# Performance work log

Measured on AMD Instinct MI355X. Metric: run time of the kernel, lower is better.

Reference implementation:

```python
import jax, jax.numpy as jnp
import numpy as np

N_WIRES = 4
N_LAYERS = 2
B = 16384
EPS = 1e-5


def apply_ry(state, wire, theta):
    # state: (B,2,2,2,2) complex64; theta: scalar or (B,)
    st = jnp.moveaxis(state, wire + 1, 1)
    half = jnp.asarray(theta) * 0.5
    c = jnp.cos(half).reshape(-1, 1, 1, 1).astype(state.dtype)
    s = jnp.sin(half).reshape(-1, 1, 1, 1).astype(state.dtype)
    n0 = c * st[:, 0] - s * st[:, 1]
    n1 = s * st[:, 0] + c * st[:, 1]
    return jnp.moveaxis(jnp.stack([n0, n1], axis=1), 1, wire + 1)


def apply_rz(state, wire, theta):
    st = jnp.moveaxis(state, wire + 1, 1)
    half = jnp.asarray(theta) * 0.5
    c = jnp.cos(half)
    s = jnp.sin(half)
    p0 = (c - 1j * s).reshape(-1, 1, 1, 1).astype(state.dtype)
    p1 = (c + 1j * s).reshape(-1, 1, 1, 1).astype(state.dtype)
    return jnp.moveaxis(jnp.stack([p0 * st[:, 0], p1 * st[:, 1]], axis=1), 1, wire + 1)


def apply_cnot(state, ctrl, tgt):
    st = jnp.moveaxis(state, (ctrl + 1, tgt + 1), (1, 2))
    # flip target where control == 1
    st = jnp.concatenate([st[:, :1], st[:, 1:, ::-1]], axis=1)
    return jnp.moveaxis(st, (1, 2), (ctrl + 1, tgt + 1))


def expect_z(state):
    probs = jnp.real(state * jnp.conj(state))  # (B,2,2,2,2)
    exps = []
    for w in range(N_WIRES):
        p = jnp.moveaxis(probs, w + 1, 1)
        exps.append((p[:, 0] - p[:, 1]).sum(axis=(1, 2, 3)))
    return jnp.stack(exps, axis=-1)  # (B,4)


def quanv(x, qparams):
    bsz = x.shape[0]
    # 2x2 patches in row-major loop order: (B, 196, 4) with [p00,p01,p10,p11]
    patches = x.reshape(bsz, 14, 2, 14, 2).transpose(0, 1, 3, 2, 4).reshape(bsz, 196, 4)
    patches = jnp.transpose(patches, (1, 0, 2))  # (196, B, 4)
    state0 = jnp.zeros((bsz, 2, 2, 2, 2), jnp.complex64).at[:, 0, 0, 0, 0].set(1.0)

    def step(state, vals):
        # NOTE: original code never resets the device between patches -> state carries over
        for i in range(N_WIRES):
            state = apply_ry(state, i, vals[:, i])
        for l in range(N_LAYERS):
            for i in range(N_WIRES):
                state = apply_ry(state, i, qparams[l, i, 0])
                state = apply_rz(state, i, qparams[l, i, 1])
            for i in range(N_WIRES - 1):
                state = apply_cnot(state, i, i + 1)
        return state, expect_z(state)

    _, meas = jax.lax.scan(step, state0, patches)  # (196, B, 4)
    return jnp.transpose(meas, (1, 0, 2)).reshape(bsz, 196 * 4)


def batchnorm(h, g, b):
    # training-mode BatchNorm1d: biased batch statistics
    m = h.mean(axis=0)
    v = h.var(axis=0)
    return g * (h - m) / jnp.sqrt(v + EPS) + b


def setup_inputs() -> dict:
    key = jax.random.key(0)
    ks = jax.random.split(key, 6)
    x = jax.random.uniform(ks[0], (B, 28, 28), dtype=jnp.float32)
    qparams = jax.random.normal(ks[1], (N_LAYERS, N_WIRES, 2), dtype=jnp.float32)
    w1 = jax.random.normal(ks[2], (256, 784), dtype=jnp.float32) * 0.03
    w2 = jax.random.normal(ks[3], (256, 256), dtype=jnp.float32) * 0.05
    w3 = jax.random.normal(ks[4], (10, 256), dtype=jnp.float32) * 0.05
    return {
        "x": x, "qparams": qparams,
        "w1": w1, "b1": jnp.zeros((256,), jnp.float32),
        "g1": jnp.ones((256,), jnp.float32), "be1": jnp.zeros((256,), jnp.float32),
        "w2": w2, "b2": jnp.zeros((256,), jnp.float32),
        "g2": jnp.ones((256,), jnp.float32), "be2": jnp.zeros((256,), jnp.float32),
        "w3": w3, "b3": jnp.zeros((10,), jnp.float32),
    }


def reference(x, qparams, w1, b1, g1, be1, w2, b2, g2, be2, w3, b3):
    feats = quanv(x, qparams)                      # (B, 784)
    h = jax.nn.relu(batchnorm(feats @ w1.T + b1, g1, be1))
    h2 = jax.nn.relu(batchnorm(h @ w2.T + b2, g2, be2)) + h
    return jax.nn.log_softmax(h2 @ w3.T + b3, axis=-1)
```

## Files before the change

### kernel.cpp

```cpp
#include <hip/hip_runtime.h>
#include <math.h>

#define BQ 16384
#define KFP 800
#define NH 256
#define NCLS 10

typedef float f32x4 __attribute__((ext_vector_type(4)));
typedef unsigned int u32x2 __attribute__((ext_vector_type(2)));
typedef unsigned int u32x4 __attribute__((ext_vector_type(4)));
typedef __bf16 bf16x8 __attribute__((ext_vector_type(8)));
typedef __bf16 bf16x4 __attribute__((ext_vector_type(4)));


template<int ST>
__device__ __forceinline__ void u_ry(float* sr, float* si, float c, float s) {
#pragma unroll
  for (int i = 0; i < 16; i++) {
    if (i & ST) continue;
    const int j = i | ST;
    const float a0r = sr[i], a0i = si[i], a1r = sr[j], a1i = si[j];
    sr[i] = c * a0r - s * a1r;  si[i] = c * a0i - s * a1i;
    sr[j] = s * a0r + c * a1r;  si[j] = s * a0i + c * a1i;
  }
}
template<int ST>
__device__ __forceinline__ void u_rz(float* sr, float* si, float c, float s) {
#pragma unroll
  for (int i = 0; i < 16; i++) {
    const float pz = (i & ST) ? s : -s;
    const float ar = sr[i], ai = si[i];
    sr[i] = c * ar - pz * ai;
    si[i] = c * ai + pz * ar;
  }
}
template<int SC, int STG>
__device__ __forceinline__ void u_cnot(float* sr, float* si) {
#pragma unroll
  for (int i = 0; i < 16; i++) {
    if (!(i & SC) || (i & STG)) continue;
    const int j = i | STG;
    float t;
    t = sr[i]; sr[i] = sr[j]; sr[j] = t;
    t = si[i]; si[i] = si[j]; si[j] = t;
  }
}

__global__ __launch_bounds__(256) void prep_kernel(
    const float* __restrict__ qp, const float* __restrict__ w1,
    const float* __restrict__ w2, __bf16* __restrict__ Abuf,
    __bf16* __restrict__ w1b, __bf16* __restrict__ w2b,
    float* __restrict__ gs1, float* __restrict__ gs2) {
  const int bid = blockIdx.x;
  const int tid = threadIdx.x;
  if (bid == 0) {
    gs1[tid] = 0.f; gs1[256 + tid] = 0.f;
    gs2[tid] = 0.f; gs2[256 + tid] = 0.f;
    __shared__ float Ur[16][16], Ui[16][16];
    if (tid < 16) {
      float sr[16], si[16];
#pragma unroll
      for (int i = 0; i < 16; i++) { sr[i] = (i == tid) ? 1.f : 0.f; si[i] = 0.f; }
#pragma unroll
      for (int l = 0; l < 2; l++) {
        { const float t = qp[l*8 + 0] * 0.5f; u_ry<8>(sr, si, cosf(t), sinf(t)); }
        { const float t = qp[l*8 + 1] * 0.5f; u_rz<8>(sr, si, cosf(t), sinf(t)); }
        { const float t = qp[l*8 + 2] * 0.5f; u_ry<4>(sr, si, cosf(t), sinf(t)); }
        { const float t = qp[l*8 + 3] * 0.5f; u_rz<4>(sr, si, cosf(t), sinf(t)); }
        { const float t = qp[l*8 + 4] * 0.5f; u_ry<2>(sr, si, cosf(t), sinf(t)); }
        { const float t = qp[l*8 + 5] * 0.5f; u_rz<2>(sr, si, cosf(t), sinf(t)); }
        { const float t = qp[l*8 + 6] * 0.5f; u_ry<1>(sr, si, cosf(t), sinf(t)); }
        { const float t = qp[l*8 + 7] * 0.5f; u_rz<1>(sr, si, cosf(t), sinf(t)); }
        u_cnot<8, 4>(sr, si);
        u_cnot<4, 2>(sr, si);
        u_cnot<2, 1>(sr, si);
      }
#pragma unroll
      for (int r = 0; r < 16; r++) { Ur[r][tid] = sr[r]; Ui[r][tid] = si[r]; }
    }
    __syncthreads();
    for (int f = tid; f < 2048; f += 256) {
      const int m   = f & 7;
      const int row = (f >> 3) & 15;
      const int kg  = (f >> 7) & 3;
      const int hl  = (f >> 9) & 1;
      const int t   = (f >> 10) & 1;
      const int k   = kg * 8 + m;
      const int ri_o  = (row >> 2) & 1;
      const int amp_o = ((row >> 3) & 1) * 8 + t * 4 + (row & 3);
      const int ri_i  = (k >> 3) & 1;
      const int amp_i = ((k >> 4) & 1) * 8 + (m >> 2) * 4 + (m & 3);
      const float u_r = Ur[amp_o][amp_i], u_i = Ui[amp_o][amp_i];
      float v = (ri_o == 0) ? ((ri_i == 0) ? u_r : -u_i)
                            : ((ri_i == 0) ? u_i : u_r);
      if (hl) {
        const __bf16 hb = (__bf16)v;
        v = v - (float)hb;
      }
      Abuf[f] = (__bf16)v;
    }
  } else if (bid <= 256) {
    const int r = bid - 1;
    for (int c = tid; c < KFP; c += 256)
      w1b[r * KFP + c] = (c < 784) ? (__bf16)w1[r * 784 + c] : (__bf16)0.f;
  } else {
    const int base = (bid - 257) * 2048 + tid * 8;
    const float4 v0 = *(const float4*)(w2 + base);
    const float4 v1 = *(const float4*)(w2 + base + 4);
    bf16x8 o = {(__bf16)v0.x, (__bf16)v0.y, (__bf16)v0.z, (__bf16)v0.w,
                (__bf16)v1.x, (__bf16)v1.y, (__bf16)v1.z, (__bf16)v1.w};
    *(bf16x8*)(w2b + base) = o;
  }
}


__device__ __forceinline__ float swz16(float v) {
  return __int_as_float(__builtin_amdgcn_ds_swizzle(__float_as_int(v), 0x401F));
}
__device__ __forceinline__ float plsum(float v) {
  const u32x2 r = __builtin_amdgcn_permlane32_swap(
      __float_as_uint(v), __float_as_uint(v), false, false);
  return __uint_as_float(r.x) + __uint_as_float(r.y);
}
__device__ __forceinline__ float plpick(float v, bool r0sel) {
  const u32x2 r = __builtin_amdgcn_permlane32_swap(
      __float_as_uint(v), __float_as_uint(v), false, false);
  return __uint_as_float(r0sel ? r.x : r.y);
}
__device__ __forceinline__ unsigned bfbits(float v) {
  return (unsigned)__builtin_bit_cast(unsigned short, (__bf16)v);
}

__global__ __launch_bounds__(256, 1) void quanv_fused(
    const float* __restrict__ x, const __bf16* __restrict__ Abuf,
    const __bf16* __restrict__ w1b, const float* __restrict__ b1,
    __bf16* __restrict__ h1p, float* __restrict__ gs1) {
  __shared__ char qlds[33792];
  const int tid = threadIdx.x;
  const int l = tid & 63;
  const int wv = tid >> 6;
  const int col = l & 15;
  const int kg = l >> 4;
  const int b = blockIdx.x * 64 + wv * 16 + col;
  const float* xb = x + (size_t)b * 784;
  const float sg0 = (l & 32) ? 1.f : -1.f;

  const u32x2 pt = __builtin_amdgcn_permlane32_swap((unsigned)l, (unsigned)l,
                                                    false, false);
  const bool p32r0 = (pt.x == (unsigned)(l ^ 32));

  const bf16x8* Ab = (const bf16x8*)Abuf;
  const bf16x8 A0h = Ab[(0 * 4 + kg) * 16 + col];
  const bf16x8 A0l = Ab[(1 * 4 + kg) * 16 + col];
  const bf16x8 A1h = Ab[(2 * 4 + kg) * 16 + col];
  const bf16x8 A1l = Ab[(3 * 4 + kg) * 16 + col];

  f32x4 c0 = {(kg == 0) ? 1.f : 0.f, 0.f, 0.f, 0.f};
  f32x4 c1 = {0.f, 0.f, 0.f, 0.f};
  const f32x4 z4 = {0.f, 0.f, 0.f, 0.f};

  u32x4 frag = {0, 0, 0, 0};
  bf16x8 bfrag[16];
  f32x4 acc[16];
#pragma unroll
  for (int nt = 0; nt < 16; nt++) acc[nt] = z4;

  auto loadB = [&](int w8) {
#pragma unroll
    for (int nt = 0; nt < 16; nt++)
      bfrag[nt] = *(const bf16x8*)(w1b + (size_t)(nt * 16 + col) * KFP +
                                   w8 * 32 + kg * 8);
  };
  auto burst = [&]() {
    const bf16x8 fa = __builtin_bit_cast(bf16x8, frag);
#pragma unroll
    for (int nt = 0; nt < 16; nt++)
      acc[nt] = __builtin_amdgcn_mfma_f32_16x16x32_bf16(fa, bfrag[nt], acc[nt], 0, 0, 0);
    frag = (u32x4){0, 0, 0, 0};
  };

  float ts0, tw1, tw2, tw3, gsc;
  auto trig = [&](float2 a, float2 b2) {
    const float h0 = a.x * 0.5f, h1 = a.y * 0.5f;
    const float h2 = b2.x * 0.5f, h3 = b2.y * 0.5f;
    const float c0_ = __cosf(h0), s0_ = __sinf(h0);
    const float c1_ = __cosf(h1), s1_ = __sinf(h1);
    const float c2_ = __cosf(h2), s2_ = __sinf(h2);
    const float c3_ = __cosf(h3), s3_ = __sinf(h3);
    ts0 = sg0 * __fdividef(s0_, c0_);
    tw1 = __fdividef(s1_, c1_);
    tw2 = __fdividef(s2_, c2_);
    tw3 = __fdividef(s3_, c3_);
    gsc = (c0_ * c1_) * (c2_ * c3_);
  };

  auto meas = [&](int mit) {
    const float sq0 = c0.x * c0.x, sq1 = c0.y * c0.y;
    const float sq2 = c0.z * c0.z, sq3 = c0.w * c0.w;
    const float sq4 = c1.x * c1.x, sq5 = c1.y * c1.y;
    const float sq6 = c1.z * c1.z, sq7 = c1.w * c1.w;
    const float s01 = sq0 + sq1, s23 = sq2 + sq3;
    const float s45 = sq4 + sq5, s67 = sq6 + sq7;
    const float d01 = sq0 - sq1, d23 = sq2 - sq3;
    const float d45 = sq4 - sq5, d67 = sq6 - sq7;
    const float z3 = (d01 + d23) + (d45 + d67);
    const float z2 = (s01 - s23) + (s45 - s67);
    const float q03 = s01 + s23, q47 = s45 + s67;
    const float z1 = q03 - q47;
    const float T  = q03 + q47;
    const float z3a = z3 + swz16(z3);
    const float z2a = z2 + swz16(z2);
    const float z1a = z1 + swz16(z1);
    const float Ta  = -sg0 * (T + swz16(T));
    const float z3f = plsum(z3a);
    const float z2f = plsum(z2a);
    const float z1f = plsum(z1a);
    const float z0f = plsum(Ta);
    const unsigned zlo = (bfbits(z1f) << 16) | bfbits(z0f);
    const unsigned zhi = (bfbits(z3f) << 16) | bfbits(z2f);
    const int p = mit & 7;
    const bool selA = ((p >> 1) == kg) & ((p & 1) == 0);
    const bool selB = ((p >> 1) == kg) & ((p & 1) == 1);
    frag.x = selA ? zlo : frag.x;
    frag.y = selA ? zhi : frag.y;
    frag.z = selB ? zlo : frag.z;
    frag.w = selB ? zhi : frag.w;
  };

  auto step = [&]() {
    float S[8] = {c0.x, c0.y, c0.z, c0.w, c1.x, c1.y, c1.z, c1.w};
#pragma unroll
    for (int j = 0; j < 4; j++) {
      const float a = S[j];
      S[j]     = fmaf(-tw1, S[4 + j], S[j]);
      S[4 + j] = fmaf( tw1, a,        S[4 + j]);
    }
#pragma unroll
    for (int base = 0; base < 8; base += 4)
#pragma unroll
      for (int j = 0; j < 2; j++) {
        const int i0 = base + j, i1 = base + j + 2;
        const float a = S[i0];
        S[i0] = fmaf(-tw2, S[i1], S[i0]);
        S[i1] = fmaf( tw2, a,     S[i1]);
      }
#pragma unroll
    for (int i0 = 0; i0 < 8; i0 += 2) {
      const float a = S[i0];
      S[i0]     = fmaf(-tw3, S[i0 + 1], S[i0]);
      S[i0 + 1] = fmaf( tw3, a,         S[i0 + 1]);
    }
#pragma unroll
    for (int i = 0; i < 8; i++) {
      const float P = plpick(S[i], p32r0);
      S[i] = fmaf(ts0, P, S[i]);
    }
    bf16x8 Bh, Bl;
#pragma unroll
    for (int i = 0; i < 8; i++) {
      const float GS = gsc * S[i];
      const __bf16 hb = (__bf16)GS;
      Bh[i] = hb;
      Bl[i] = (__bf16)(GS - (float)hb);
    }
    f32x4 p0 = __builtin_amdgcn_mfma_f32_16x16x32_bf16(A0h, Bh, z4, 0, 0, 0);
    f32x4 q0 = __builtin_amdgcn_mfma_f32_16x16x32_bf16(A0l, Bh, z4, 0, 0, 0);
    q0 = __builtin_amdgcn_mfma_f32_16x16x32_bf16(A0h, Bl, q0, 0, 0, 0);
    f32x4 p1 = __builtin_amdgcn_mfma_f32_16x16x32_bf16(A1h, Bh, z4, 0, 0, 0);
    f32x4 q1 = __builtin_amdgcn_mfma_f32_16x16x32_bf16(A1l, Bh, z4, 0, 0, 0);
    q1 = __builtin_amdgcn_mfma_f32_16x16x32_bf16(A1h, Bl, q1, 0, 0, 0);
    c0 = p0 + q0;
    c1 = p1 + q1;
  };

  loadB(0);
  float2 t0 = *(const float2*)(xb);
  float2 t1 = *(const float2*)(xb + 28);
  trig(t0, t1);
  t0 = *(const float2*)(xb + 2);
  t1 = *(const float2*)(xb + 30);
  step();
  trig(t0, t1);
  t0 = *(const float2*)(xb + 4);
  t1 = *(const float2*)(xb + 32);
  int nrr = 0, ncc = 3;

  for (int it = 1; it < 196; ++it) {
    const float* np = (it < 194) ? (xb + 56 * nrr + 2 * ncc) : xb;
    const float2 n0 = *(const float2*)np;
    const float2 n1 = *(const float2*)(np + 28);
    ncc++;
    if (ncc == 14) { ncc = 0; nrr++; }

    meas(it - 1);
    if ((it & 7) == 0) {
      burst();
      loadB(it >> 3);
    }
    step();
    trig(t0, t1);
    t0 = n0; t1 = n1;
  }
  meas(195);
  burst();

  float bv[16];
#pragma unroll
  for (int nt = 0; nt < 16; nt++) bv[nt] = b1[nt * 16 + col];
  float* sredS = (float*)qlds;
  float* sredQ = sredS + 4096;
#pragma unroll
  for (int nt = 0; nt < 16; nt++) {
    float s = 0.f, q = 0.f;
#pragma unroll
    for (int r = 0; r < 4; r++) {
      const float v = acc[nt][r] + bv[nt];
      s += v; q += v * v;
    }
    sredS[(wv * 4 + kg) * 256 + nt * 16 + col] = s;
    sredQ[(wv * 4 + kg) * 256 + nt * 16 + col] = q;
  }
  __syncthreads();
  {
    float s = 0.f, q = 0.f;
#pragma unroll
    for (int r = 0; r < 16; r++) {
      s += sredS[r * 256 + tid];
      q += sredQ[r * 256 + tid];
    }
    atomicAdd(&gs1[tid * 2], s);
    atomicAdd(&gs1[tid * 2 + 1], q);
  }
  __syncthreads();

  __bf16* tile = (__bf16*)qlds;
#pragma unroll
  for (int nt = 0; nt < 16; nt++)
#pragma unroll
    for (int r = 0; r < 4; r++)
      tile[(wv * 16 + kg * 4 + r) * 264 + nt * 16 + col] =
          (__bf16)(acc[nt][r] + bv[nt]);
  __syncthreads();
  for (int pass = 0; pass < 8; pass++) {
    const int idx = pass * 256 + tid;
    const int row = idx >> 5, c8 = idx & 31;
    const bf16x8 vv = *(const bf16x8*)&tile[row * 264 + c8 * 8];
    *(bf16x8*)(h1p + ((size_t)(blockIdx.x * 64 + row)) * 256 + c8 * 8) = vv;
  }
}

#define GBM 128
#define GBN 64
#define GBK 32

__device__ __forceinline__ void gld16(const void* g, void* l) {
  __builtin_amdgcn_global_load_lds(
      (const __attribute__((address_space(1))) unsigned int*)g,
      (__attribute__((address_space(3))) unsigned int*)l, 16, 0, 0);
}

__global__ __launch_bounds__(256) void gemm_bf16_nt(
    const __bf16* __restrict__ A, const __bf16* __restrict__ B,
    const float* __restrict__ bias, __bf16* __restrict__ C,
    int M, int N, int K, float* __restrict__ gstats) {
  __shared__ char lds[24576];
  const int tid = threadIdx.x;
  const int nwg = gridDim.x;
  const int sid = (blockIdx.x & 7) * (nwg >> 3) + (blockIdx.x >> 3);
  const int bm = (sid >> 2) * GBM;
  const int bn = (sid & 3) * GBN;
  const int NK = K / GBK;
  const size_t lda = (size_t)K * 2;

  const int srow = tid >> 2;
  const int lc16 = tid & 3;
  const int ag0 = lc16 ^ ((srow >> 1) & 3);
  const int ag1 = lc16 ^ (((srow + 64) >> 1) & 3);
  const char* a0p = (const char*)A + (size_t)(bm + srow) * lda + ag0 * 16;
  const char* a1p = (const char*)A + (size_t)(bm + 64 + srow) * lda + ag1 * 16;
  const char* b0p = (const char*)B + (size_t)(bn + srow) * lda + ag0 * 16;

  const int wid = tid >> 6, lane = tid & 63;
  const int wr = wid >> 1, wc = wid & 1;
  const int ln15 = lane & 15, ln4 = lane >> 4;
  int aoff[4], boff[2];
#pragma unroll
  for (int m = 0; m < 4; m++) {
    const int row = wr * 64 + m * 16 + ln15;
    aoff[m] = row * 64 + ((ln4 ^ ((row >> 1) & 3)) * 16);
  }
#pragma unroll
  for (int n = 0; n < 2; n++) {
    const int row = wc * 32 + n * 16 + ln15;
    boff[n] = 16384 + row * 64 + ((ln4 ^ ((row >> 1) & 3)) * 16);
  }

  f32x4 acc[4][2];
#pragma unroll
  for (int m = 0; m < 4; m++)
#pragma unroll
    for (int n = 0; n < 2; n++) acc[m][n] = (f32x4){0.f, 0.f, 0.f, 0.f};

  auto stage = [&](int buf, int kt) {
    const size_t kb = (size_t)kt * GBK * 2;
    char* as = lds + buf * 8192 + tid * 16;
    char* bs = lds + 16384 + buf * 4096 + tid * 16;
    gld16(a0p + kb, as);
    gld16(a1p + kb, as + 4096);
    gld16(b0p + kb, bs);
  };

  stage(0, 0);
  for (int kt = 0; kt < NK; kt++) {
    __syncthreads();
    if (kt + 1 < NK) stage((kt + 1) & 1, kt + 1);
    const int ab = (kt & 1) * 8192, bb = (kt & 1) * 4096;
    bf16x8 af[4], bfr[2];
#pragma unroll
    for (int m = 0; m < 4; m++) af[m] = *(const bf16x8*)(lds + ab + aoff[m]);
#pragma unroll
    for (int n = 0; n < 2; n++) bfr[n] = *(const bf16x8*)(lds + bb + boff[n]);
#pragma unroll
    for (int m = 0; m < 4; m++)
#pragma unroll
      for (int n = 0; n < 2; n++)
        acc[m][n] = __builtin_amdgcn_mfma_f32_16x16x32_bf16(af[m], bfr[n], acc[m][n], 0, 0, 0);
  }

  float csum[2], csq[2];
#pragma unroll
  for (int n = 0; n < 2; n++) {
    const int ccol = bn + wc * 32 + n * 16 + ln15;
    const float bv = bias[ccol];
    float s = 0.f, ss = 0.f;
#pragma unroll
    for (int m = 0; m < 4; m++) {
      const int crow = bm + wr * 64 + m * 16 + ln4 * 4;
#pragma unroll
      for (int r = 0; r < 4; r++) {
        const float v = acc[m][n][r] + bv;
        C[(size_t)(crow + r) * N + ccol] = (__bf16)v;
        s += v; ss += v * v;
      }
    }
    csum[n] = s; csq[n] = ss;
  }
  __syncthreads();
  float* sred = (float*)lds;
#pragma unroll
  for (int n = 0; n < 2; n++) {
    const int slot = wid * 128 + ln4 * 32 + n * 16 + ln15;
    sred[slot] = csum[n];
    sred[512 + slot] = csq[n];
  }
  __syncthreads();
  if (tid < 128) {
    const int colb = tid & 63, which = tid >> 6;
    const int wcc = colb >> 5, c31 = colb & 31;
    float a = 0.f;
    const int base = which * 512 + c31;
#pragma unroll
    for (int w2_ = 0; w2_ < 2; w2_++)
#pragma unroll
      for (int l4 = 0; l4 < 4; l4++)
        a += sred[base + (w2_ * 2 + wcc) * 128 + l4 * 32];
    atomicAdd(&gstats[(bn + colb) * 2 + which], a);
  }
}

__global__ __launch_bounds__(256) void bn1_relu(
    const __bf16* __restrict__ h1p, __bf16* __restrict__ h1b,
    const float* __restrict__ gstats, const float* __restrict__ g,
    const float* __restrict__ be) {
  __shared__ float as[NH], cs[NH];
  {
    const int t = threadIdx.x;
    const float s = gstats[t * 2], ss = gstats[t * 2 + 1];
    const float mean = s * (1.f / 16384.f);
    const float var = ss * (1.f / 16384.f) - mean * mean;
    const float a = g[t] * rsqrtf(var + 1e-5f);
    as[t] = a;
    cs[t] = be[t] - mean * a;
  }
  __syncthreads();
  const size_t i = (size_t)blockIdx.x * 256 + threadIdx.x;
  const bf16x8 v = *(const bf16x8*)(h1p + i * 8);
  const int colb = (int)((i * 8) & (NH - 1));
  bf16x8 o;
#pragma unroll
  for (int j = 0; j < 8; j++)
    o[j] = (__bf16)fmaxf(fmaf((float)v[j], as[colb + j], cs[colb + j]), 0.f);
  *(bf16x8*)(h1b + i * 8) = o;
}

__global__ __launch_bounds__(256) void tail_fused(
    const __bf16* __restrict__ h2b, const __bf16* __restrict__ h1b,
    const float* __restrict__ gstats, const float* __restrict__ g,
    const float* __restrict__ be, const float* __restrict__ w3,
    const float* __restrict__ b3, float* __restrict__ out) {
  __shared__ float w3s[NCLS * NH];
  __shared__ float as[NH], cs[NH];
  for (int i = threadIdx.x; i < NCLS * NH; i += 256) w3s[i] = w3[i];
  {
    const int t = threadIdx.x;
    const float s = gstats[t * 2], ss = gstats[t * 2 + 1];
    const float mean = s * (1.f / 16384.f);
    const float var = ss * (1.f / 16384.f) - mean * mean;
    const float a = g[t] * rsqrtf(var + 1e-5f);
    as[t] = a;
    cs[t] = be[t] - mean * a;
  }
  __syncthreads();

  const int m = blockIdx.x * 256 + threadIdx.x;
  const __bf16* hr = h2b + (size_t)m * NH;
  const __bf16* rr = h1b + (size_t)m * NH;
  float acc[NCLS];
#pragma unroll
  for (int n = 0; n < NCLS; n++) acc[n] = b3[n];

  for (int k = 0; k < NH; k += 8) {
    const bf16x8 hv = *(const bf16x8*)(hr + k);
    const bf16x8 rv = *(const bf16x8*)(rr + k);
    float v[8];
#pragma unroll
    for (int j = 0; j < 8; j++)
      v[j] = fmaxf(fmaf((float)hv[j], as[k + j], cs[k + j]), 0.f) + (float)rv[j];
#pragma unroll
    for (int n = 0; n < NCLS; n++) {
      float d = 0.f;
#pragma unroll
      for (int j = 0; j < 8; j++) d = fmaf(v[j], w3s[n * NH + k + j], d);
      acc[n] += d;
    }
  }

  float mx = acc[0];
#pragma unroll
  for (int n = 1; n < NCLS; n++) mx = fmaxf(mx, acc[n]);
  float se = 0.f;
#pragma unroll
  for (int n = 0; n < NCLS; n++) se += expf(acc[n] - mx);
  const float lse = logf(se) + mx;
#pragma unroll
  for (int n = 0; n < NCLS; n++) out[(size_t)m * NCLS + n] = acc[n] - lse;
}

extern "C" void kernel_launch(void* const* d_in, const int* in_sizes, int n_in,
                              void* d_out, int out_size, void* d_ws, size_t ws_size,
                              hipStream_t stream) {
  const float* x   = (const float*)d_in[0];
  const float* qp  = (const float*)d_in[1];
  const float* w1  = (const float*)d_in[2];
  const float* b1  = (const float*)d_in[3];
  const float* g1  = (const float*)d_in[4];
  const float* be1 = (const float*)d_in[5];
  const float* w2  = (const float*)d_in[6];
  const float* b2  = (const float*)d_in[7];
  const float* g2  = (const float*)d_in[8];
  const float* be2 = (const float*)d_in[9];
  const float* w3  = (const float*)d_in[10];
  const float* b3  = (const float*)d_in[11];
  float* out = (float*)d_out;

  char* w = (char*)d_ws;
  __bf16* h1p   = (__bf16*)w;
  __bf16* h1b   = (__bf16*)(w + 8388608);
  __bf16* h2b   = (__bf16*)(w + 16777216);
  __bf16* w1b   = (__bf16*)(w + 25165824);
  __bf16* w2b   = (__bf16*)(w + 25575424);
  float*  gs1   = (float*)(w + 25706496);
  float*  gs2   = (float*)(w + 25708544);
  __bf16* Abuf  = (__bf16*)(w + 25710592);

  prep_kernel<<<289, 256, 0, stream>>>(qp, w1, w2, Abuf, w1b, w2b, gs1, gs2);

  quanv_fused<<<BQ / 64, 256, 0, stream>>>(x, Abuf, w1b, b1, h1p, gs1);

  bn1_relu<<<(BQ * NH / 8) / 256, 256, 0, stream>>>(h1p, h1b, gs1, g1, be1);

  gemm_bf16_nt<<<(BQ / GBM) * (NH / GBN), 256, 0, stream>>>(
      h1b, w2b, b2, h2b, BQ, NH, NH, gs2);

  tail_fused<<<BQ / 256, 256, 0, stream>>>(h2b, h1b, gs2, g2, be2, w3, b3, out);
}
```

Before: 194.5 us.

## Fuse BN1+ReLU into quanv kernel via cooperative grid sync

The quanv kernel now keeps its pre-BN tile in LDS, performs a grid-wide cooperative sync once every block has accumulated its batch statistics, then applies batchnorm and ReLU before writing h1b directly. This removes the separate bn1_relu launch and the round trip of the intermediate h1p buffer through global memory. The kernel is launched cooperatively with 256 blocks, which requires all blocks to be co-resident, and the grid sync adds a global barrier. It also swaps the ds_swizzle reductions for permlane16_swap where the compiler supports it.

```diff
diff --git a/kernel.cpp b/kernel.cpp
--- a/kernel.cpp
+++ b/kernel.cpp
@@ -1,5 +1,8 @@
 #include <hip/hip_runtime.h>
+#include <hip/hip_cooperative_groups.h>
 #include <math.h>
+
+namespace cg = cooperative_groups;
 
 #define BQ 16384
 #define KFP 800
@@ -11,7 +14,6 @@
 typedef unsigned int u32x4 __attribute__((ext_vector_type(4)));
 typedef __bf16 bf16x8 __attribute__((ext_vector_type(8)));
 typedef __bf16 bf16x4 __attribute__((ext_vector_type(4)));
-
 
 template<int ST>
 __device__ __forceinline__ void u_ry(float* sr, float* si, float c, float s) {
@@ -127,6 +129,20 @@
       __float_as_uint(v), __float_as_uint(v), false, false);
   return __uint_as_float(r0sel ? r.x : r.y);
 }
+#if defined(__has_builtin)
+#if __has_builtin(__builtin_amdgcn_permlane16_swap)
+#define HAVE_PL16 1
+#endif
+#endif
+__device__ __forceinline__ float pl16sum(float v) {
+#ifdef HAVE_PL16
+  const u32x2 r = __builtin_amdgcn_permlane16_swap(
+      __float_as_uint(v), __float_as_uint(v), false, false);
+  return __uint_as_float(r.x) + __uint_as_float(r.y);
+#else
+  return v + swz16(v);
+#endif
+}
 __device__ __forceinline__ unsigned bfbits(float v) {
   return (unsigned)__builtin_bit_cast(unsigned short, (__bf16)v);
 }
@@ -134,8 +150,9 @@
 __global__ __launch_bounds__(256, 1) void quanv_fused(
     const float* __restrict__ x, const __bf16* __restrict__ Abuf,
     const __bf16* __restrict__ w1b, const float* __restrict__ b1,
-    __bf16* __restrict__ h1p, float* __restrict__ gs1) {
-  __shared__ char qlds[33792];
+    const float* __restrict__ g1, const float* __restrict__ be1,
+    float* __restrict__ gs1, __bf16* __restrict__ h1b) {
+  __shared__ char qlds[35840];
   const int tid = threadIdx.x;
   const int l = tid & 63;
   const int wv = tid >> 6;
@@ -208,10 +225,10 @@
     const float q03 = s01 + s23, q47 = s45 + s67;
     const float z1 = q03 - q47;
     const float T  = q03 + q47;
-    const float z3a = z3 + swz16(z3);
-    const float z2a = z2 + swz16(z2);
-    const float z1a = z1 + swz16(z1);
-    const float Ta  = -sg0 * (T + swz16(T));
+    const float z3a = pl16sum(z3);
+    const float z2a = pl16sum(z2);
+    const float z1a = pl16sum(z1);
+    const float Ta  = -sg0 * pl16sum(T);
     const float z3f = plsum(z3a);
     const float z2f = plsum(z2a);
     const float z1f = plsum(z1a);
@@ -340,12 +357,36 @@
     for (int r = 0; r < 4; r++)
       tile[(wv * 16 + kg * 4 + r) * 264 + nt * 16 + col] =
           (__bf16)(acc[nt][r] + bv[nt]);
+
+  __threadfence();
+  cg::this_grid().sync();
+
+  float* asl = (float*)(qlds + 33792);
+  float* csl = asl + 256;
+  {
+    const float s = gs1[tid * 2], ss = gs1[tid * 2 + 1];
+    const float mean = s * (1.f / 16384.f);
+    const float var = ss * (1.f / 16384.f) - mean * mean;
+    const float a = g1[tid] * rsqrtf(var + 1e-5f);
+    asl[tid] = a;
+    csl[tid] = be1[tid] - mean * a;
+  }
   __syncthreads();
   for (int pass = 0; pass < 8; pass++) {
     const int idx = pass * 256 + tid;
     const int row = idx >> 5, c8 = idx & 31;
     const bf16x8 vv = *(const bf16x8*)&tile[row * 264 + c8 * 8];
-    *(bf16x8*)(h1p + ((size_t)(blockIdx.x * 64 + row)) * 256 + c8 * 8) = vv;
+    const float4 a0 = *(const float4*)&asl[c8 * 8];
+    const float4 a1 = *(const float4*)&asl[c8 * 8 + 4];
+    const float4 cc0 = *(const float4*)&csl[c8 * 8];
+    const float4 cc1 = *(const float4*)&csl[c8 * 8 + 4];
+    const float av[8] = {a0.x, a0.y, a0.z, a0.w, a1.x, a1.y, a1.z, a1.w};
+    const float cv[8] = {cc0.x, cc0.y, cc0.z, cc0.w, cc1.x, cc1.y, cc1.z, cc1.w};
+    bf16x8 o;
+#pragma unroll
+    for (int j = 0; j < 8; j++)
+      o[j] = (__bf16)fmaxf(fmaf((float)vv[j], av[j], cv[j]), 0.f);
+    *(bf16x8*)(h1b + ((size_t)(blockIdx.x * 64 + row)) * 256 + c8 * 8) = o;
   }
 }
 
@@ -466,31 +507,6 @@
         a += sred[base + (w2_ * 2 + wcc) * 128 + l4 * 32];
     atomicAdd(&gstats[(bn + colb) * 2 + which], a);
   }
-}
-
-__global__ __launch_bounds__(256) void bn1_relu(
-    const __bf16* __restrict__ h1p, __bf16* __restrict__ h1b,
-    const float* __restrict__ gstats, const float* __restrict__ g,
-    const float* __restrict__ be) {
-  __shared__ float as[NH], cs[NH];
-  {
-    const int t = threadIdx.x;
-    const float s = gstats[t * 2], ss = gstats[t * 2 + 1];
-    const float mean = s * (1.f / 16384.f);
-    const float var = ss * (1.f / 16384.f) - mean * mean;
-    const float a = g[t] * rsqrtf(var + 1e-5f);
-    as[t] = a;
-    cs[t] = be[t] - mean * a;
-  }
-  __syncthreads();
-  const size_t i = (size_t)blockIdx.x * 256 + threadIdx.x;
-  const bf16x8 v = *(const bf16x8*)(h1p + i * 8);
-  const int colb = (int)((i * 8) & (NH - 1));
-  bf16x8 o;
-#pragma unroll
-  for (int j = 0; j < 8; j++)
-    o[j] = (__bf16)fmaxf(fmaf((float)v[j], as[colb + j], cs[colb + j]), 0.f);
-  *(bf16x8*)(h1b + i * 8) = o;
 }
 
 __global__ __launch_bounds__(256) void tail_fused(
@@ -564,20 +580,22 @@
   float* out = (float*)d_out;
 
   char* w = (char*)d_ws;
-  __bf16* h1p   = (__bf16*)w;
-  __bf16* h1b   = (__bf16*)(w + 8388608);
-  __bf16* h2b   = (__bf16*)(w + 16777216);
-  __bf16* w1b   = (__bf16*)(w + 25165824);
-  __bf16* w2b   = (__bf16*)(w + 25575424);
-  float*  gs1   = (float*)(w + 25706496);
-  float*  gs2   = (float*)(w + 25708544);
-  __bf16* Abuf  = (__bf16*)(w + 25710592);
+  __bf16* h1b   = (__bf16*)w;
+  __bf16* h2b   = (__bf16*)(w + 8388608);
+  __bf16* w1b   = (__bf16*)(w + 16777216);
+  __bf16* w2b   = (__bf16*)(w + 17186816);
+  float*  gs1   = (float*)(w + 17317888);
+  float*  gs2   = (float*)(w + 17319936);
+  __bf16* Abuf  = (__bf16*)(w + 17321984);
 
   prep_kernel<<<289, 256, 0, stream>>>(qp, w1, w2, Abuf, w1b, w2b, gs1, gs2);
 
-  quanv_fused<<<BQ / 64, 256, 0, stream>>>(x, Abuf, w1b, b1, h1p, gs1);
-
-  bn1_relu<<<(BQ * NH / 8) / 256, 256, 0, stream>>>(h1p, h1b, gs1, g1, be1);
+  {
+    void* kargs[] = {(void*)&x, (void*)&Abuf, (void*)&w1b, (void*)&b1,
+                     (void*)&g1, (void*)&be1, (void*)&gs1, (void*)&h1b};
+    hipLaunchCooperativeKernel((const void*)quanv_fused, dim3(BQ / 64),
+                               dim3(256), kargs, 0, stream);
+  }
 
   gemm_bf16_nt<<<(BQ / GBM) * (NH / GBN), 256, 0, stream>>>(
       h1b, w2b, b2, h2b, BQ, NH, NH, gs2);
```

Result: slower. 237.8 us (+22.3%).
